# Optimization experiments

Measured on AMD Instinct MI355X. Metric: run time of the kernel, lower is better.

Reference implementation:

```python
import jax, jax.numpy as jnp
import numpy as np

B, SD, SE = 4, 2048, 2048
HID, HID_ = 300, 512
N_HEADS = 8


def setup_inputs() -> dict:
    key = jax.random.key(0)
    ks = jax.random.split(key, 7)
    en = jax.random.normal(ks[0], (B, SE, HID), dtype=jnp.float32)
    de = jax.random.normal(ks[1], (B, SD, HID), dtype=jnp.float32)
    mask = jax.random.randint(ks[2], (1, 1, SD, SE), 0, 2).astype(jnp.bool_)
    WQ = jax.random.normal(ks[3], (HID, HID_), dtype=jnp.float32)
    WK = jax.random.normal(ks[4], (HID, HID_), dtype=jnp.float32)
    WV = jax.random.normal(ks[5], (HID, HID_), dtype=jnp.float32)
    WO = jax.random.normal(ks[6], (HID_, HID), dtype=jnp.float32)
    return {"en": en, "de": de, "mask": mask, "WQ": WQ, "WK": WK, "WV": WV, "WO": WO}


def reference(en, de, mask, WQ, WK, WV, WO):
    # Faithful to the torch module (dropout in eval mode => identity).
    d_k = de.shape[-1]  # NOTE: original scales by sqrt(hidden_dim)=sqrt(300), not head_dim
    b_d, s_d = de.shape[0], de.shape[1]
    b_e, s_e = en.shape[0], en.shape[1]
    # head axis is the LAST axis of the reshape (size 8), exactly as the original view/permute
    q = jnp.transpose((de @ WQ).reshape(b_d, s_d, -1, N_HEADS), (3, 0, 1, 2))  # [8,B,Sd,64]
    k = jnp.transpose((en @ WK).reshape(b_e, s_e, -1, N_HEADS), (3, 0, 2, 1))  # [8,B,64,Se]
    v = jnp.transpose((en @ WV).reshape(b_e, s_e, -1, N_HEADS), (3, 0, 1, 2))  # [8,B,Se,64]
    e = jnp.matmul(q, k) / jnp.sqrt(jnp.asarray(d_k, dtype=q.dtype))           # [8,B,Sd,Se]
    e = jnp.where(mask, jnp.asarray(-1e9, dtype=e.dtype), e)
    alpha = jax.nn.softmax(e, axis=3)
    head3 = jnp.matmul(alpha, v)                                               # [8,B,Sd,64]
    # torch.cat((head3[0],...,head3[7]), 2) == move head axis into feature concat order
    a = jnp.concatenate([head3[h] for h in range(N_HEADS)], axis=2)            # [B,Sd,512]
    return a @ WO                                                              # [B,Sd,300]
```

## Files before the change

### kernel.cpp

```cpp
#include <hip/hip_runtime.h>
#include <hip/hip_bf16.h>
#include <math.h>

#define B_      4
#define SD_     2048
#define SE_     2048
#define HIDIN   300
#define HIDMID  512
#define NH      8
#define DH      64
#define ESZ     ((size_t)4194304)
#define BUFB    24576

typedef __attribute__((ext_vector_type(8))) short          s16x8;
typedef __attribute__((ext_vector_type(8))) unsigned short u16x8;
typedef __attribute__((ext_vector_type(4))) unsigned short u16x4;
typedef __attribute__((ext_vector_type(4))) float          f32x4;

#define MFMA16 __builtin_amdgcn_mfma_f32_16x16x32_bf16

#define QSCALE  0.0832940411f
#define NEGL   -1.4426950e9f
#define DEFER_THR 24.0f

__device__ __forceinline__ unsigned short f2bf(float f) {
    unsigned int u = __float_as_uint(f);
    u += 0x7fffu + ((u >> 16) & 1u);
    return (unsigned short)(u >> 16);
}
__device__ __forceinline__ float bf2f(unsigned short s) {
    return __uint_as_float((unsigned int)s << 16);
}
__device__ __forceinline__ void gload16(const void* g, void* l) {
    __builtin_amdgcn_global_load_lds(
        (const __attribute__((address_space(1))) void*)g,
        (__attribute__((address_space(3))) void*)l, 16, 0, 0);
}
__device__ __forceinline__ float fexp2(float x) {
#if __has_builtin(__builtin_amdgcn_exp2f)
    return __builtin_amdgcn_exp2f(x);
#else
    return exp2f(x);
#endif
}

#define OF_QH   ((size_t)0)
#define OF_QL   (ESZ)
#define OF_KH   (2*ESZ)
#define OF_KL   (3*ESZ)
#define OF_VT   (4*ESZ)
#define OF_CA   (5*ESZ)
#define OF_CW   (OF_CA + 10485760)
#define OF_WOT  (OF_CW + 983040)

__global__ __launch_bounds__(256) void bias_kernel(const int* __restrict__ mask,
                                                   unsigned int* __restrict__ BiasT)
{
    const int idx = blockIdx.x * 256 + threadIdx.x;
    const int q = idx >> 5, tile = idx & 31;
    const int* __restrict__ mrow = mask + (size_t)q * SE_ + tile * 64;
    const unsigned int NEGB = (unsigned int)f2bf(NEGL);
    const int qblk = q >> 4, qlo = q & 15;
#pragma unroll
    for (int g = 0; g < 4; ++g) {
        unsigned int w[8];
#pragma unroll
        for (int sub = 0; sub < 4; ++sub) {
            const int4 mm = *(const int4*)(mrow + sub * 16 + g * 4);
            w[sub * 2]     = (mm.x ? NEGB : 0u) | ((mm.y ? NEGB : 0u) << 16);
            w[sub * 2 + 1] = (mm.z ? NEGB : 0u) | ((mm.w ? NEGB : 0u) << 16);
        }
        unsigned int* dst = BiasT +
            ((((size_t)qblk * 32 + tile) * 4 + g) * 16 + qlo) * 8;
        *(uint4*)dst       = make_uint4(w[0], w[1], w[2], w[3]);
        *(uint4*)(dst + 4) = make_uint4(w[4], w[5], w[6], w[7]);
    }
}

__global__ __launch_bounds__(256) void convA_kernel(
    const float* __restrict__ de, const float* __restrict__ en,
    unsigned short* __restrict__ CA)
{
    const int idx = blockIdx.x * 256 + threadIdx.x;
    const int mat = blockIdx.y;
    const float* __restrict__ A = mat ? en : de;
    unsigned short* __restrict__ H = CA + (size_t)mat * 5242880;
    unsigned short* __restrict__ L = H + 2621440;
    const int row = idx / 10, ch = idx - row * 10;
    float v[32];
    if (ch < 9) {
#pragma unroll
        for (int i = 0; i < 8; ++i) {
            const float4 f = *(const float4*)(A + (size_t)row * 300 + ch * 32 + i * 4);
            v[i*4+0] = f.x; v[i*4+1] = f.y; v[i*4+2] = f.z; v[i*4+3] = f.w;
        }
    } else {
#pragma unroll
        for (int i = 0; i < 32; ++i) {
            const int k = 288 + i;
            v[i] = (k < 300) ? A[(size_t)row * 300 + k] : 0.f;
        }
    }
    const int r128 = row & 127;
    const int xr = (r128 >> 1) & 3;
    const size_t tb = ((size_t)(row >> 7) * 10 + ch) * 4096 + r128 * 32;
#pragma unroll
    for (int sub = 0; sub < 4; ++sub) {
        const int slot = sub ^ xr;
        u16x8 hv, lv;
#pragma unroll
        for (int e = 0; e < 8; ++e) {
            const float f = v[sub * 8 + e];
            const unsigned short h = f2bf(f);
            hv[e] = h; lv[e] = f2bf(f - bf2f(h));
        }
        *(u16x8*)(H + tb + slot * 8) = hv;
        *(u16x8*)(L + tb + slot * 8) = lv;
    }
}

__global__ __launch_bounds__(256) void convW_kernel(
    const float* __restrict__ WQ, const float* __restrict__ WK,
    const float* __restrict__ WV, const float* __restrict__ WO,
    unsigned short* __restrict__ CW, unsigned short* __restrict__ WOT)
{
    const int idx = blockIdx.x * 256 + threadIdx.x;
    if (idx < 122880) {
        const int which = idx / 40960;
        const int rem = idx - which * 40960;
        const int k = rem >> 7;
        const int n0 = (rem & 127) * 4;
        const float* __restrict__ W = which == 0 ? WQ : (which == 1 ? WK : WV);
        unsigned short* __restrict__ H = CW + (size_t)which * 327680;
        unsigned short* __restrict__ L = H + 163840;
        const float sc = (which == 0) ? QSCALE : 1.f;
        float4 w = make_float4(0.f, 0.f, 0.f, 0.f);
        if (k < 300) w = *(const float4*)(W + (size_t)k * 512 + n0);
        const float wv4[4] = {w.x * sc, w.y * sc, w.z * sc, w.w * sc};
        const int ch = k >> 5, kk = k & 31;
#pragma unroll
        for (int j = 0; j < 4; ++j) {
            const int n = n0 + j, ntile = n >> 7, nr = n & 127;
            const size_t o = ((size_t)(ntile * 10 + ch) * 128 + nr) * 32
                           + (((kk >> 3) ^ ((nr >> 1) & 3)) << 3) + (kk & 7);
            const unsigned short h = f2bf(wv4[j]);
            H[o] = h;
            if (which < 2) L[o] = f2bf(wv4[j] - bf2f(h));
        }
    } else {
        const int idx2 = idx - 122880;
        const int k = idx2 / 96, n4 = idx2 - k * 96;
        const int n0 = n4 * 4;
        float4 w = make_float4(0.f, 0.f, 0.f, 0.f);
        if (n0 < 300) w = *(const float4*)(WO + (size_t)k * 300 + n0);
        const float wv4[4] = {w.x, w.y, w.z, w.w};
        const int ch = k >> 5, kk = k & 31;
#pragma unroll
        for (int j = 0; j < 4; ++j) {
            const int n = n0 + j, ntile = n >> 7, nr = n & 127;
            const size_t o = ((size_t)(ntile * 16 + ch) * 128 + nr) * 32
                           + (((kk >> 3) ^ ((nr >> 1) & 3)) << 3) + (kk & 7);
            WOT[o] = f2bf(wv4[j]);
        }
    }
}

__global__ __launch_bounds__(256) void proj_qk_kernel(
    const unsigned short* __restrict__ CA, const unsigned short* __restrict__ CW,
    unsigned short* __restrict__ Qh, unsigned short* __restrict__ Ql,
    unsigned short* __restrict__ KhT, unsigned short* __restrict__ KlT)
{
    const int lin = blockIdx.x;
    const int which = lin >> 8;
    const int t = lin & 255;
    const int stile = (t & 7) | ((t >> 5) << 3);
    const int jtile = (t >> 3) & 3;
    const int tid = threadIdx.x, wv = tid >> 6, lane = tid & 63;
    const int li = lane & 15, g = lane >> 4;
    const int wr = wv >> 1, wc = wv & 1;

    __shared__ __align__(16) char LBp[65536];

    const unsigned short* __restrict__ pAh =
        CA + (size_t)which * 5242880 + (size_t)stile * 40960 + tid * 8;
    const unsigned short* __restrict__ pAl = pAh + 2621440;
    const unsigned short* __restrict__ pWh =
        CW + (size_t)which * 327680 + (size_t)jtile * 40960 + tid * 8;
    const unsigned short* __restrict__ pWl = pWh + 163840;

#define STAGEP(ch, bofs) {                                                    \
        char* db = LBp + (bofs) + wv * 1024;                                  \
        const size_t co = (size_t)(ch) * 4096;                                \
        gload16(pAh + co,        db);                                         \
        gload16(pAh + co + 2048, db + 4096);                                  \
        gload16(pAl + co,        db + 8192);                                  \
        gload16(pAl + co + 2048, db + 12288);                                 \
        gload16(pWh + co,        db + 16384);                                 \
        gload16(pWh + co + 2048, db + 20480);                                 \
        gload16(pWl + co,        db + 24576);                                 \
        gload16(pWl + co + 2048, db + 28672);                                 \
    }

    int offA[4], offW[4];
#pragma unroll
    for (int ssub = 0; ssub < 4; ++ssub) {
        const int r = wr * 64 + ssub * 16 + li;
        offA[ssub] = r * 64 + ((g ^ ((r >> 1) & 3)) << 4);
    }
#pragma unroll
    for (int jsub = 0; jsub < 4; ++jsub) {
        const int n = wc * 64 + jsub * 16 + li;
        offW[jsub] = n * 64 + ((g ^ ((n >> 1) & 3)) << 4);
    }

    f32x4 acc[4][4];
#pragma unroll
    for (int i = 0; i < 4; ++i)
#pragma unroll
        for (int j = 0; j < 4; ++j) acc[i][j] = (f32x4){0.f, 0.f, 0.f, 0.f};

    STAGEP(0, 0)
    __syncthreads();

#pragma unroll 1
    for (int ch = 0; ch < 10; ++ch) {
        const int bofs = (ch & 1) * 32768;
        if (ch < 9) STAGEP(ch + 1, bofs ^ 32768)
        const char* bp = LBp + bofs;
        s16x8 ah[4], al[4], wh[4], wl[4];
#pragma unroll
        for (int ssub = 0; ssub < 4; ++ssub) {
            ah[ssub] = *(const s16x8*)(bp + offA[ssub]);
            al[ssub] = *(const s16x8*)(bp + 8192 + offA[ssub]);
        }
#pragma unroll
        for (int jsub = 0; jsub < 4; ++jsub) {
            wh[jsub] = *(const s16x8*)(bp + 16384 + offW[jsub]);
            wl[jsub] = *(const s16x8*)(bp + 24576 + offW[jsub]);
        }
        __builtin_amdgcn_s_setprio(1);
#pragma unroll
        for (int ssub = 0; ssub < 4; ++ssub)
#pragma unroll
            for (int jsub = 0; jsub < 4; ++jsub) {
                acc[ssub][jsub] = MFMA16(ah[ssub], wh[jsub], acc[ssub][jsub], 0, 0, 0);
                acc[ssub][jsub] = MFMA16(ah[ssub], wl[jsub], acc[ssub][jsub], 0, 0, 0);
                acc[ssub][jsub] = MFMA16(al[ssub], wh[jsub], acc[ssub][jsub], 0, 0, 0);
            }
        __builtin_amdgcn_s_setprio(0);
        __syncthreads();
    }
#undef STAGEP

    const int jgbase = jtile * 128 + wc * 64 + li;
    const int sbase0 = stile * 128 + wr * 64 + 4 * g;
#pragma unroll
    for (int jsub = 0; jsub < 4; ++jsub) {
        const int jgg = jgbase + jsub * 16;
        const int d = jgg >> 3, hh = jgg & 7;
#pragma unroll
        for (int ssub = 0; ssub < 4; ++ssub) {
            const f32x4 v = acc[ssub][jsub];
            const int sg0 = sbase0 + ssub * 16;
            const int bbv = sg0 >> 11;
            const int bhn = bbv * 8 + hh;
            const int sl0 = sg0 & 2047;
            if (which == 0) {
                const size_t o = ((size_t)bhn * 2048 + sl0) * 64 + d;
#pragma unroll
                for (int r = 0; r < 4; ++r) {
                    const float val = v[r];
                    const unsigned short hi = f2bf(val);
                    Qh[o + r * 64] = hi;
                    Ql[o + r * 64] = f2bf(val - bf2f(hi));
                }
            } else {
                const int tile = sl0 >> 6, tt0 = sl0 & 63;
                const size_t tb = ((size_t)(bhn * 32 + tile)) << 12;
#pragma unroll
                for (int r = 0; r < 4; ++r) {
                    const int tt = tt0 + r;
                    const size_t o = tb + tt * 64 + (((d >> 3) ^ (tt & 7)) << 3) + (d & 7);
                    const float val = v[r];
                    const unsigned short hi = f2bf(val);
                    KhT[o] = hi;
                    KlT[o] = f2bf(val - bf2f(hi));
                }
            }
        }
    }
}

__global__ __launch_bounds__(256) void proj_v_kernel(
    const unsigned short* __restrict__ CA, const unsigned short* __restrict__ CW,
    unsigned short* __restrict__ VtT)
{
    const int t = blockIdx.x;
    const int stile = (t & 7) | ((t >> 5) << 3);
    const int jtile = (t >> 3) & 3;
    const int tid = threadIdx.x, wv = tid >> 6, lane = tid & 63;
    const int li = lane & 15, g = lane >> 4;
    const int wr = wv >> 1, wc = wv & 1;

    __shared__ __align__(16) char LBv[32768];

    const unsigned short* __restrict__ pAh =
        CA + (size_t)1 * 5242880 + (size_t)stile * 40960 + tid * 8;
    const unsigned short* __restrict__ pWh =
        CW + (size_t)2 * 327680 + (size_t)jtile * 40960 + tid * 8;

#define STAGEV(ch, bofs) {                                                    \
        char* db = LBv + (bofs) + wv * 1024;                                  \
        const size_t co = (size_t)(ch) * 4096;                                \
        gload16(pAh + co,        db);                                         \
        gload16(pAh + co + 2048, db + 4096);                                  \
        gload16(pWh + co,        db + 8192);                                  \
        gload16(pWh + co + 2048, db + 12288);                                 \
    }

    int offA[4], offW[4];
#pragma unroll
    for (int ssub = 0; ssub < 4; ++ssub) {
        const int r = wr * 64 + ssub * 16 + li;
        offA[ssub] = r * 64 + ((g ^ ((r >> 1) & 3)) << 4);
    }
#pragma unroll
    for (int jsub = 0; jsub < 4; ++jsub) {
        const int n = wc * 64 + jsub * 16 + li;
        offW[jsub] = 8192 + n * 64 + ((g ^ ((n >> 1) & 3)) << 4);
    }

    f32x4 acc[4][4];
#pragma unroll
    for (int i = 0; i < 4; ++i)
#pragma unroll
        for (int j = 0; j < 4; ++j) acc[i][j] = (f32x4){0.f, 0.f, 0.f, 0.f};

    STAGEV(0, 0)
    __syncthreads();

#pragma unroll 1
    for (int ch = 0; ch < 10; ++ch) {
        const int bofs = (ch & 1) * 16384;
        if (ch < 9) STAGEV(ch + 1, bofs ^ 16384)
        const char* bp = LBv + bofs;
        s16x8 ah[4], wh[4];
#pragma unroll
        for (int ssub = 0; ssub < 4; ++ssub)
            ah[ssub] = *(const s16x8*)(bp + offA[ssub]);
#pragma unroll
        for (int jsub = 0; jsub < 4; ++jsub)
            wh[jsub] = *(const s16x8*)(bp + offW[jsub]);
        __builtin_amdgcn_s_setprio(1);
#pragma unroll
        for (int ssub = 0; ssub < 4; ++ssub)
#pragma unroll
            for (int jsub = 0; jsub < 4; ++jsub)
                acc[ssub][jsub] = MFMA16(ah[ssub], wh[jsub], acc[ssub][jsub], 0, 0, 0);
        __builtin_amdgcn_s_setprio(0);
        __syncthreads();
    }
#undef STAGEV

    const int jgbase = jtile * 128 + wc * 64 + li;
    const int sbase0 = stile * 128 + wr * 64 + 4 * g;
#pragma unroll
    for (int jsub = 0; jsub < 4; ++jsub) {
        const int jgg = jgbase + jsub * 16;
        const int d = jgg >> 3, hh = jgg & 7;
#pragma unroll
        for (int ssub = 0; ssub < 4; ++ssub) {
            const f32x4 v = acc[ssub][jsub];
            const int sg0 = sbase0 + ssub * 16;
            const int bbv = sg0 >> 11;
            const int bhn = bbv * 8 + hh;
            const int sl0 = sg0 & 2047;
            const int tile = sl0 >> 6, tin0 = sl0 & 63;
            const size_t tb = ((size_t)(bhn * 32 + tile)) << 12;
            const int blk = tin0 >> 5, gg2 = (tin0 >> 2) & 3, half = (tin0 >> 4) & 1;
            const size_t o = tb + (size_t)d * 64
                           + ((((blk << 2) | gg2) ^ (d & 7)) << 3) + half * 4;
            u16x4 pk;
#pragma unroll
            for (int r = 0; r < 4; ++r) pk[r] = f2bf(v[r]);
            *(u16x4*)(VtT + o) = pk;
        }
    }
}

__global__ __launch_bounds__(512, 4) void attn_mfma_kernel(
    const unsigned short* __restrict__ Qh, const unsigned short* __restrict__ Ql,
    const unsigned short* __restrict__ KhT, const unsigned short* __restrict__ KlT,
    const unsigned short* __restrict__ VtT, const unsigned int* __restrict__ BiasT,
    unsigned short* __restrict__ AOb)
{
    const int lin = blockIdx.x + 16 * blockIdx.y;
    const int qt = (lin >> 3) & 15;
    const int bh = (lin & 7) + ((lin >> 7) << 3);
    const int bb = bh >> 3, hh = bh & 7;
    const int tid = threadIdx.x;
    const int wv = tid >> 6, lane = tid & 63;
    const int g = lane >> 4, li = lane & 15;
    const int q = qt * 128 + wv * 16 + li;

    __shared__ __align__(16) char LB[3 * BUFB];

    const size_t qoff = ((size_t)bh * SD_ + q) * DH + 8 * g;
    const s16x8 qh0 = *(const s16x8*)(Qh + qoff);
    const s16x8 qh1 = *(const s16x8*)(Qh + qoff + 32);
    const s16x8 ql0 = *(const s16x8*)(Ql + qoff);
    const s16x8 ql1 = *(const s16x8*)(Ql + qoff + 32);

    const unsigned short* __restrict__ sKh = KhT + ((size_t)bh << 17) + tid * 8;
    const unsigned short* __restrict__ sKl = KlT + ((size_t)bh << 17) + tid * 8;
    const unsigned short* __restrict__ sVt = VtT + ((size_t)bh << 17) + tid * 8;

    const int base0 = li * 128 + ((g ^ (li & 7)) << 4);
    const int base1 = li * 128 + (((4 + g) ^ (li & 7)) << 4);

    const size_t bbase = (size_t)(qt * 8 + wv) * 16384 + g * 128 + li * 8;

#define BIASLOAD(T, RA, RB) {                                                 \
        const uint4* p = (const uint4*)(BiasT + bbase + (size_t)(T) * 512);   \
        RA = p[0]; RB = p[1];                                                 \
    }

#define STAGE(tile, boff)                                                     \
    {                                                                         \
        char* db = LB + (boff) + wv * 1024;                                   \
        const size_t toff = (size_t)(tile) << 12;                             \
        gload16(sKh + toff, db);                                              \
        gload16(sKl + toff, db + 8192);                                       \
        gload16(sVt + toff, db + 16384);                                      \
    }

    float m = -INFINITY;
    f32x4 O[4], lacc;
#pragma unroll
    for (int i = 0; i < 4; ++i) O[i] = (f32x4){0.f, 0.f, 0.f, 0.f};
    lacc = (f32x4){0.f, 0.f, 0.f, 0.f};

    s16x8 ones;
#pragma unroll
    for (int i = 0; i < 8; ++i) ones[i] = (short)0x3F80;

    uint4 cBA, cBB, nBA, nBB;

#define UNPK(W, S, sub, cbase)                                                \
        S[sub][cbase]     = __uint_as_float((W) << 16);                       \
        S[sub][cbase + 1] = __uint_as_float((W) & 0xFFFF0000u);

#define ITER(IT, CBA_, CBB_, NBA_, NBB_)                                      \
    {                                                                         \
        BIASLOAD(((IT) + 1) & 31, NBA_, NBB_)                                 \
        STAGE(((IT) + 2) & 31, cs)                                            \
        f32x4 s[4];                                                           \
        UNPK(CBA_.x, s, 0, 0) UNPK(CBA_.y, s, 0, 2)                           \
        UNPK(CBA_.z, s, 1, 0) UNPK(CBA_.w, s, 1, 2)                           \
        UNPK(CBB_.x, s, 2, 0) UNPK(CBB_.y, s, 2, 2)                           \
        UNPK(CBB_.z, s, 3, 0) UNPK(CBB_.w, s, 3, 2)                           \
        __builtin_amdgcn_s_setprio(1);                                        \
        _Pragma("unroll")                                                     \
        for (int sub = 0; sub < 4; ++sub) {                                   \
            const s16x8 kh0 = *(const s16x8*)(LB + cc + base0 + sub * 2048);  \
            const s16x8 kh1 = *(const s16x8*)(LB + cc + base1 + sub * 2048);  \
            const s16x8 kl0 = *(const s16x8*)(LB + cc + base0 + 8192 + sub * 2048); \
            const s16x8 kl1 = *(const s16x8*)(LB + cc + base1 + 8192 + sub * 2048); \
            s[sub] = MFMA16(kh0, qh0, s[sub], 0, 0, 0);                       \
            s[sub] = MFMA16(kh0, ql0, s[sub], 0, 0, 0);                       \
            s[sub] = MFMA16(kl0, qh0, s[sub], 0, 0, 0);                       \
            s[sub] = MFMA16(kh1, qh1, s[sub], 0, 0, 0);                       \
            s[sub] = MFMA16(kh1, ql1, s[sub], 0, 0, 0);                       \
            s[sub] = MFMA16(kl1, qh1, s[sub], 0, 0, 0);                       \
        }                                                                     \
        __builtin_amdgcn_s_setprio(0);                                        \
        float x0 = fmaxf(fmaxf(s[0][0], s[0][1]), s[0][2]);                   \
        float x1 = fmaxf(fmaxf(s[0][3], s[1][0]), s[1][1]);                   \
        float x2 = fmaxf(fmaxf(s[1][2], s[1][3]), s[2][0]);                   \
        float x3 = fmaxf(fmaxf(s[2][1], s[2][2]), s[2][3]);                   \
        float x4 = fmaxf(fmaxf(s[3][0], s[3][1]), s[3][2]);                   \
        float tmax = fmaxf(fmaxf(fmaxf(x0, x1), fmaxf(x2, x3)),               \
                           fmaxf(x4, s[3][3]));                               \
        if (!__all(tmax <= m + DEFER_THR)) {                                  \
            float r = fmaxf(tmax, __shfl_xor(tmax, 16));                      \
            r = fmaxf(r, __shfl_xor(r, 32));                                  \
            const float mn  = fmaxf(m, r);                                    \
            const float scl = fexp2(m - mn);                                  \
            m = mn;                                                           \
            _Pragma("unroll")                                                 \
            for (int i = 0; i < 4; ++i) O[i] *= scl;                          \
            lacc *= scl;                                                      \
        }                                                                     \
        _Pragma("unroll")                                                     \
        for (int sub = 0; sub < 4; ++sub)                                     \
            _Pragma("unroll")                                                 \
            for (int c = 0; c < 4; ++c)                                       \
                s[sub][c] = fexp2(s[sub][c] - m);                             \
        union { s16x8 v; unsigned int w[4]; } P0, P1;                         \
        asm("v_cvt_pk_bf16_f32 %0, %1, %2" : "=v"(P0.w[0]) : "v"(s[0][0]), "v"(s[0][1])); \
        asm("v_cvt_pk_bf16_f32 %0, %1, %2" : "=v"(P0.w[1]) : "v"(s[0][2]), "v"(s[0][3])); \
        asm("v_cvt_pk_bf16_f32 %0, %1, %2" : "=v"(P0.w[2]) : "v"(s[1][0]), "v"(s[1][1])); \
        asm("v_cvt_pk_bf16_f32 %0, %1, %2" : "=v"(P0.w[3]) : "v"(s[1][2]), "v"(s[1][3])); \
        asm("v_cvt_pk_bf16_f32 %0, %1, %2" : "=v"(P1.w[0]) : "v"(s[2][0]), "v"(s[2][1])); \
        asm("v_cvt_pk_bf16_f32 %0, %1, %2" : "=v"(P1.w[1]) : "v"(s[2][2]), "v"(s[2][3])); \
        asm("v_cvt_pk_bf16_f32 %0, %1, %2" : "=v"(P1.w[2]) : "v"(s[3][0]), "v"(s[3][1])); \
        asm("v_cvt_pk_bf16_f32 %0, %1, %2" : "=v"(P1.w[3]) : "v"(s[3][2]), "v"(s[3][3])); \
        __builtin_amdgcn_s_setprio(1);                                        \
        _Pragma("unroll")                                                     \
        for (int dsub = 0; dsub < 4; ++dsub) {                                \
            const s16x8 vf0 = *(const s16x8*)(LB + cc + base0 + 16384 + dsub * 2048); \
            const s16x8 vf1 = *(const s16x8*)(LB + cc + base1 + 16384 + dsub * 2048); \
            O[dsub] = MFMA16(vf0, P0.v, O[dsub], 0, 0, 0);                    \
            O[dsub] = MFMA16(vf1, P1.v, O[dsub], 0, 0, 0);                    \
        }                                                                     \
        lacc = MFMA16(ones, P0.v, lacc, 0, 0, 0);                             \
        lacc = MFMA16(ones, P1.v, lacc, 0, 0, 0);                             \
        __builtin_amdgcn_s_setprio(0);                                        \
        asm volatile("s_waitcnt vmcnt(3)" ::: "memory");                      \
        __builtin_amdgcn_s_barrier();                                         \
        __builtin_amdgcn_sched_barrier(0);                                    \
        cc += BUFB; if (cc == 3 * BUFB) cc = 0;                               \
        cs += BUFB; if (cs == 3 * BUFB) cs = 0;                               \
    }

    int cc = 0, cs = 2 * BUFB;

    BIASLOAD(0, cBA, cBB)
    STAGE(0, 0)
    STAGE(1, BUFB)
    asm volatile("s_waitcnt vmcnt(3)" ::: "memory");
    __builtin_amdgcn_s_barrier();
    __builtin_amdgcn_sched_barrier(0);

#pragma unroll 1
    for (int it = 0; it < 32; it += 2) {
        ITER(it,     cBA, cBB, nBA, nBB)
        ITER(it + 1, nBA, nBB, cBA, cBB)
    }

    const float rl = 1.f / lacc[0];
    const int row = bb * 2048 + q;
    const int r128 = row & 127;
    const int xr = (r128 >> 1) & 3;
    unsigned short* __restrict__ ab = AOb + ((size_t)(row >> 7)) * 65536
                                    + r128 * 32 + (g & 1) * 4;
#pragma unroll
    for (int dsub = 0; dsub < 4; ++dsub) {
        const f32x4 o = O[dsub] * rl;
        const int ch = hh * 2 + (dsub >> 1);
        const int slot = ((dsub & 1) * 2 + (g >> 1)) ^ xr;
        u16x4 pk;
#pragma unroll
        for (int c = 0; c < 4; ++c) pk[c] = f2bf(o[c]);
        *(u16x4*)(ab + (size_t)ch * 4096 + slot * 8) = pk;
    }
#undef STAGE
#undef BIASLOAD
#undef UNPK
#undef ITER
}

__global__ __launch_bounds__(256) void epi_mfma_kernel(
    const unsigned short* __restrict__ AOb, const unsigned short* __restrict__ WOT,
    float* __restrict__ out)
{
    const int stile = blockIdx.x, jtile = blockIdx.y;
    const int tid = threadIdx.x, wv = tid >> 6, lane = tid & 63;
    const int li = lane & 15, g = lane >> 4;

    __shared__ __align__(16) char LBe[24576];

    const unsigned short* __restrict__ pA =
        AOb + (size_t)(stile >> 1) * 65536 + (stile & 1) * 2048 + tid * 8;
    const unsigned short* __restrict__ pW = WOT + (size_t)jtile * 65536 + tid * 8;

#define STAGEE(ch, bofs) {                                                    \
        char* dbA = LBe + (bofs) + wv * 1024;                                 \
        const size_t co = (size_t)(ch) * 4096;                                \
        gload16(pA + co,        dbA);                                         \
        gload16(pW + co,        dbA + 4096);                                  \
        gload16(pW + co + 2048, dbA + 8192);                                  \
    }

    int offA[4], offW[2];
#pragma unroll
    for (int ssub = 0; ssub < 4; ++ssub) {
        const int r = ssub * 16 + li;
        offA[ssub] = r * 64 + ((g ^ ((r >> 1) & 3)) << 4);
    }
#pragma unroll
    for (int jsub = 0; jsub < 2; ++jsub) {
        const int n = wv * 32 + jsub * 16 + li;
        offW[jsub] = 4096 + n * 64 + ((g ^ ((n >> 1) & 3)) << 4);
    }

    f32x4 acc[4][2];
#pragma unroll
    for (int i = 0; i < 4; ++i)
#pragma unroll
        for (int j = 0; j < 2; ++j) acc[i][j] = (f32x4){0.f, 0.f, 0.f, 0.f};

    STAGEE(0, 0)
    __syncthreads();

#pragma unroll 1
    for (int ch = 0; ch < 16; ++ch) {
        const int bofs = (ch & 1) * 12288;
        if (ch < 15) STAGEE(ch + 1, bofs ^ 12288)
        const char* bp = LBe + bofs;
        s16x8 ah[4], wh[2];
#pragma unroll
        for (int ssub = 0; ssub < 4; ++ssub)
            ah[ssub] = *(const s16x8*)(bp + offA[ssub]);
#pragma unroll
        for (int jsub = 0; jsub < 2; ++jsub)
            wh[jsub] = *(const s16x8*)(bp + offW[jsub]);
        __builtin_amdgcn_s_setprio(1);
#pragma unroll
        for (int ssub = 0; ssub < 4; ++ssub)
#pragma unroll
            for (int jsub = 0; jsub < 2; ++jsub)
                acc[ssub][jsub] = MFMA16(ah[ssub], wh[jsub], acc[ssub][jsub], 0, 0, 0);
        __builtin_amdgcn_s_setprio(0);
        __syncthreads();
    }
#undef STAGEE

    const int nbase = jtile * 128 + wv * 32 + li;
    const int rbase = stile * 64 + 4 * g;
#pragma unroll
    for (int jsub = 0; jsub < 2; ++jsub) {
        const int o = nbase + jsub * 16;
        if (o < HIDIN) {
#pragma unroll
            for (int ssub = 0; ssub < 4; ++ssub) {
                const f32x4 v = acc[ssub][jsub];
                const int r0 = rbase + ssub * 16;
#pragma unroll
                for (int r = 0; r < 4; ++r)
                    out[(size_t)(r0 + r) * HIDIN + o] = v[r];
            }
        }
    }
}

extern "C" void kernel_launch(void* const* d_in, const int* in_sizes, int n_in,
                              void* d_out, int out_size, void* d_ws, size_t ws_size,
                              hipStream_t stream)
{
    const float* en  = (const float*)d_in[0];
    const float* de  = (const float*)d_in[1];
    const int*   mask = (const int*)d_in[2];
    const float* WQ  = (const float*)d_in[3];
    const float* WK  = (const float*)d_in[4];
    const float* WV  = (const float*)d_in[5];
    const float* WO  = (const float*)d_in[6];
    float* out = (float*)d_out;

    unsigned short* ws2 = (unsigned short*)d_ws;
    unsigned short* Qh  = ws2 + OF_QH;
    unsigned short* Ql  = ws2 + OF_QL;
    unsigned short* KhT = ws2 + OF_KH;
    unsigned short* KlT = ws2 + OF_KL;
    unsigned short* VtT = ws2 + OF_VT;
    unsigned short* CA  = ws2 + OF_CA;
    unsigned short* CW  = ws2 + OF_CW;
    unsigned short* WOT = ws2 + OF_WOT;
    unsigned short* AOb = CA;
    unsigned int*  BiasT = (unsigned int*)(CA + 4194304);

    convA_kernel<<<dim3(320, 2), 256, 0, stream>>>(de, en, CA);
    convW_kernel<<<dim3(672), 256, 0, stream>>>(WQ, WK, WV, WO, CW, WOT);
    proj_qk_kernel<<<dim3(512), 256, 0, stream>>>(CA, CW, Qh, Ql, KhT, KlT);
    proj_v_kernel<<<dim3(256), 256, 0, stream>>>(CA, CW, VtT);
    bias_kernel<<<dim3(256), 256, 0, stream>>>(mask, BiasT);
    attn_mfma_kernel<<<dim3(16, 32), 512, 0, stream>>>(Qh, Ql, KhT, KlT, VtT, BiasT, AOb);
    epi_mfma_kernel<<<dim3(128, 3), 256, 0, stream>>>(AOb, WOT, out);
}
```

Baseline: 176.0 us.

## Split attention over key range with two query rows per wave and merge pass

Adds an attention kernel that splits the key sequence into two halves across blocks. Each wave processes two 16-row query groups, so every K/V tile loaded into LDS feeds twice the MFMA work. The kernel writes partial outputs plus per-row max and sum to workspace, and a new merge kernel combines them into the blocked layout that the epilogue kernel expects. In exchange, each wave holds more registers, partial results make an extra round trip through memory, and the path needs a larger workspace, falling back to the original kernel when the workspace is too small.

```diff
diff --git a/kernel.cpp b/kernel.cpp
--- a/kernel.cpp
+++ b/kernel.cpp
@@ -52,6 +52,8 @@
 #define OF_CA   (5*ESZ)
 #define OF_CW   (OF_CA + 10485760)
 #define OF_WOT  (OF_CW + 983040)
+#define OF_PART (OF_WOT + 196608)
+#define WS_NEED_SPLIT ((size_t)(OF_PART + 8388608 + 524288) * 2)
 
 __global__ __launch_bounds__(256) void bias_kernel(const int* __restrict__ mask,
                                                    unsigned int* __restrict__ BiasT)
@@ -424,7 +426,6 @@
         const uint4* p = (const uint4*)(BiasT + bbase + (size_t)(T) * 512);   \
         RA = p[0]; RB = p[1];                                                 \
     }
-
 #define STAGE(tile, boff)                                                     \
     {                                                                         \
         char* db = LB + (boff) + wv * 1024;                                   \
@@ -560,6 +561,252 @@
 #undef ITER
 }
 
+__global__ __launch_bounds__(512, 4) void attn2_kernel(
+    const unsigned short* __restrict__ Qh, const unsigned short* __restrict__ Ql,
+    const unsigned short* __restrict__ KhT, const unsigned short* __restrict__ KlT,
+    const unsigned short* __restrict__ VtT, const unsigned int* __restrict__ BiasT,
+    unsigned short* __restrict__ Opart, float2* __restrict__ ML)
+{
+    const int lin = blockIdx.x + 16 * blockIdx.y;
+    const int qt2 = (lin >> 3) & 15;
+    const int qt = qt2 >> 1, split = qt2 & 1;
+    const int bh = (lin & 7) | ((lin >> 7) << 3);
+    const int tid = threadIdx.x;
+    const int wv = tid >> 6, lane = tid & 63;
+    const int g = lane >> 4, li = lane & 15;
+    const int q0 = qt * 256 + wv * 16 + li;
+    const int tbase = split * 16;
+
+    __shared__ __align__(16) char LB[3 * BUFB];
+
+    const size_t qoff = ((size_t)bh * SD_ + q0) * DH + 8 * g;
+    const s16x8 qh0_0 = *(const s16x8*)(Qh + qoff);
+    const s16x8 qh1_0 = *(const s16x8*)(Qh + qoff + 32);
+    const s16x8 ql0_0 = *(const s16x8*)(Ql + qoff);
+    const s16x8 ql1_0 = *(const s16x8*)(Ql + qoff + 32);
+    const s16x8 qh0_1 = *(const s16x8*)(Qh + qoff + 8192);
+    const s16x8 qh1_1 = *(const s16x8*)(Qh + qoff + 8224);
+    const s16x8 ql0_1 = *(const s16x8*)(Ql + qoff + 8192);
+    const s16x8 ql1_1 = *(const s16x8*)(Ql + qoff + 8224);
+
+    const unsigned short* __restrict__ sKh = KhT + ((size_t)bh << 17) + tid * 8;
+    const unsigned short* __restrict__ sKl = KlT + ((size_t)bh << 17) + tid * 8;
+    const unsigned short* __restrict__ sVt = VtT + ((size_t)bh << 17) + tid * 8;
+
+    const int base0 = li * 128 + ((g ^ (li & 7)) << 4);
+    const int base1 = li * 128 + (((4 + g) ^ (li & 7)) << 4);
+
+    const size_t bb0 = (size_t)(qt * 16 + wv) * 16384 + g * 128 + li * 8;
+    const size_t bb1 = bb0 + 131072;
+
+#define STAGE2(tile, boff)                                                    \
+    {                                                                         \
+        char* db = LB + (boff) + wv * 1024;                                   \
+        const size_t toff = (size_t)(tile) << 12;                             \
+        gload16(sKh + toff, db);                                              \
+        gload16(sKl + toff, db + 8192);                                       \
+        gload16(sVt + toff, db + 16384);                                      \
+    }
+#define UNPK2(W, S, sub, cbase)                                               \
+        S[sub][cbase]     = __uint_as_float((W) << 16);                       \
+        S[sub][cbase + 1] = __uint_as_float((W) & 0xFFFF0000u);
+
+    float m0 = -INFINITY, m1 = -INFINITY;
+    f32x4 O0[4], O1[4], lacc0, lacc1;
+#pragma unroll
+    for (int i = 0; i < 4; ++i) {
+        O0[i] = (f32x4){0.f, 0.f, 0.f, 0.f};
+        O1[i] = (f32x4){0.f, 0.f, 0.f, 0.f};
+    }
+    lacc0 = (f32x4){0.f, 0.f, 0.f, 0.f};
+    lacc1 = (f32x4){0.f, 0.f, 0.f, 0.f};
+
+    s16x8 ones;
+#pragma unroll
+    for (int i = 0; i < 8; ++i) ones[i] = (short)0x3F80;
+
+    int cc = 0, cs = 2 * BUFB;
+    STAGE2(tbase, 0)
+    STAGE2(tbase + 1, BUFB)
+    asm volatile("s_waitcnt vmcnt(3)" ::: "memory");
+    __builtin_amdgcn_s_barrier();
+    __builtin_amdgcn_sched_barrier(0);
+
+#pragma unroll 1
+    for (int it = 0; it < 16; ++it) {
+        const uint4* pb0 = (const uint4*)(BiasT + bb0 + (size_t)(tbase + it) * 512);
+        const uint4 bA0 = pb0[0], bB0 = pb0[1];
+        const uint4* pb1 = (const uint4*)(BiasT + bb1 + (size_t)(tbase + it) * 512);
+        const uint4 bA1 = pb1[0], bB1 = pb1[1];
+        STAGE2(tbase + ((it + 2) & 15), cs)
+
+        f32x4 s0[4], s1[4];
+        UNPK2(bA0.x, s0, 0, 0) UNPK2(bA0.y, s0, 0, 2)
+        UNPK2(bA0.z, s0, 1, 0) UNPK2(bA0.w, s0, 1, 2)
+        UNPK2(bB0.x, s0, 2, 0) UNPK2(bB0.y, s0, 2, 2)
+        UNPK2(bB0.z, s0, 3, 0) UNPK2(bB0.w, s0, 3, 2)
+        UNPK2(bA1.x, s1, 0, 0) UNPK2(bA1.y, s1, 0, 2)
+        UNPK2(bA1.z, s1, 1, 0) UNPK2(bA1.w, s1, 1, 2)
+        UNPK2(bB1.x, s1, 2, 0) UNPK2(bB1.y, s1, 2, 2)
+        UNPK2(bB1.z, s1, 3, 0) UNPK2(bB1.w, s1, 3, 2)
+
+        __builtin_amdgcn_s_setprio(1);
+#pragma unroll
+        for (int sub = 0; sub < 4; ++sub) {
+            const s16x8 kh0 = *(const s16x8*)(LB + cc + base0 + sub * 2048);
+            const s16x8 kh1 = *(const s16x8*)(LB + cc + base1 + sub * 2048);
+            const s16x8 kl0 = *(const s16x8*)(LB + cc + base0 + 8192 + sub * 2048);
+            const s16x8 kl1 = *(const s16x8*)(LB + cc + base1 + 8192 + sub * 2048);
+            s0[sub] = MFMA16(kh0, qh0_0, s0[sub], 0, 0, 0);
+            s0[sub] = MFMA16(kh0, ql0_0, s0[sub], 0, 0, 0);
+            s0[sub] = MFMA16(kl0, qh0_0, s0[sub], 0, 0, 0);
+            s0[sub] = MFMA16(kh1, qh1_0, s0[sub], 0, 0, 0);
+            s0[sub] = MFMA16(kh1, ql1_0, s0[sub], 0, 0, 0);
+            s0[sub] = MFMA16(kl1, qh1_0, s0[sub], 0, 0, 0);
+            s1[sub] = MFMA16(kh0, qh0_1, s1[sub], 0, 0, 0);
+            s1[sub] = MFMA16(kh0, ql0_1, s1[sub], 0, 0, 0);
+            s1[sub] = MFMA16(kl0, qh0_1, s1[sub], 0, 0, 0);
+            s1[sub] = MFMA16(kh1, qh1_1, s1[sub], 0, 0, 0);
+            s1[sub] = MFMA16(kh1, ql1_1, s1[sub], 0, 0, 0);
+            s1[sub] = MFMA16(kl1, qh1_1, s1[sub], 0, 0, 0);
+        }
+        __builtin_amdgcn_s_setprio(0);
+
+        float t0, t1;
+        {
+            float a = fmaxf(fmaxf(s0[0][0], s0[0][1]), s0[0][2]);
+            float b = fmaxf(fmaxf(s0[0][3], s0[1][0]), s0[1][1]);
+            float c = fmaxf(fmaxf(s0[1][2], s0[1][3]), s0[2][0]);
+            float d = fmaxf(fmaxf(s0[2][1], s0[2][2]), s0[2][3]);
+            float e = fmaxf(fmaxf(s0[3][0], s0[3][1]), s0[3][2]);
+            t0 = fmaxf(fmaxf(fmaxf(a, b), fmaxf(c, d)), fmaxf(e, s0[3][3]));
+        }
+        {
+            float a = fmaxf(fmaxf(s1[0][0], s1[0][1]), s1[0][2]);
+            float b = fmaxf(fmaxf(s1[0][3], s1[1][0]), s1[1][1]);
+            float c = fmaxf(fmaxf(s1[1][2], s1[1][3]), s1[2][0]);
+            float d = fmaxf(fmaxf(s1[2][1], s1[2][2]), s1[2][3]);
+            float e = fmaxf(fmaxf(s1[3][0], s1[3][1]), s1[3][2]);
+            t1 = fmaxf(fmaxf(fmaxf(a, b), fmaxf(c, d)), fmaxf(e, s1[3][3]));
+        }
+        const int okd = (t0 <= m0 + DEFER_THR) && (t1 <= m1 + DEFER_THR);
+        if (!__all(okd)) {
+            float r0 = fmaxf(t0, __shfl_xor(t0, 16));
+            r0 = fmaxf(r0, __shfl_xor(r0, 32));
+            float r1 = fmaxf(t1, __shfl_xor(t1, 16));
+            r1 = fmaxf(r1, __shfl_xor(r1, 32));
+            const float mn0 = fmaxf(m0, r0), mn1 = fmaxf(m1, r1);
+            const float sc0 = fexp2(m0 - mn0), sc1 = fexp2(m1 - mn1);
+            m0 = mn0; m1 = mn1;
+#pragma unroll
+            for (int i = 0; i < 4; ++i) { O0[i] *= sc0; O1[i] *= sc1; }
+            lacc0 *= sc0; lacc1 *= sc1;
+        }
+#pragma unroll
+        for (int sub = 0; sub < 4; ++sub)
+#pragma unroll
+            for (int c = 0; c < 4; ++c) {
+                s0[sub][c] = fexp2(s0[sub][c] - m0);
+                s1[sub][c] = fexp2(s1[sub][c] - m1);
+            }
+
+        union { s16x8 v; unsigned int w[4]; } P00, P10, P01, P11;
+        asm("v_cvt_pk_bf16_f32 %0, %1, %2" : "=v"(P00.w[0]) : "v"(s0[0][0]), "v"(s0[0][1]));
+        asm("v_cvt_pk_bf16_f32 %0, %1, %2" : "=v"(P00.w[1]) : "v"(s0[0][2]), "v"(s0[0][3]));
+        asm("v_cvt_pk_bf16_f32 %0, %1, %2" : "=v"(P00.w[2]) : "v"(s0[1][0]), "v"(s0[1][1]));
+        asm("v_cvt_pk_bf16_f32 %0, %1, %2" : "=v"(P00.w[3]) : "v"(s0[1][2]), "v"(s0[1][3]));
+        asm("v_cvt_pk_bf16_f32 %0, %1, %2" : "=v"(P10.w[0]) : "v"(s0[2][0]), "v"(s0[2][1]));
+        asm("v_cvt_pk_bf16_f32 %0, %1, %2" : "=v"(P10.w[1]) : "v"(s0[2][2]), "v"(s0[2][3]));
+        asm("v_cvt_pk_bf16_f32 %0, %1, %2" : "=v"(P10.w[2]) : "v"(s0[3][0]), "v"(s0[3][1]));
+        asm("v_cvt_pk_bf16_f32 %0, %1, %2" : "=v"(P10.w[3]) : "v"(s0[3][2]), "v"(s0[3][3]));
+        asm("v_cvt_pk_bf16_f32 %0, %1, %2" : "=v"(P01.w[0]) : "v"(s1[0][0]), "v"(s1[0][1]));
+        asm("v_cvt_pk_bf16_f32 %0, %1, %2" : "=v"(P01.w[1]) : "v"(s1[0][2]), "v"(s1[0][3]));
+        asm("v_cvt_pk_bf16_f32 %0, %1, %2" : "=v"(P01.w[2]) : "v"(s1[1][0]), "v"(s1[1][1]));
+        asm("v_cvt_pk_bf16_f32 %0, %1, %2" : "=v"(P01.w[3]) : "v"(s1[1][2]), "v"(s1[1][3]));
+        asm("v_cvt_pk_bf16_f32 %0, %1, %2" : "=v"(P11.w[0]) : "v"(s1[2][0]), "v"(s1[2][1]));
+        asm("v_cvt_pk_bf16_f32 %0, %1, %2" : "=v"(P11.w[1]) : "v"(s1[2][2]), "v"(s1[2][3]));
+        asm("v_cvt_pk_bf16_f32 %0, %1, %2" : "=v"(P11.w[2]) : "v"(s1[3][0]), "v"(s1[3][1]));
+        asm("v_cvt_pk_bf16_f32 %0, %1, %2" : "=v"(P11.w[3]) : "v"(s1[3][2]), "v"(s1[3][3]));
+
+        __builtin_amdgcn_s_setprio(1);
+#pragma unroll
+        for (int dsub = 0; dsub < 4; ++dsub) {
+            const s16x8 vf0 = *(const s16x8*)(LB + cc + base0 + 16384 + dsub * 2048);
+            const s16x8 vf1 = *(const s16x8*)(LB + cc + base1 + 16384 + dsub * 2048);
+            O0[dsub] = MFMA16(vf0, P00.v, O0[dsub], 0, 0, 0);
+            O0[dsub] = MFMA16(vf1, P10.v, O0[dsub], 0, 0, 0);
+            O1[dsub] = MFMA16(vf0, P01.v, O1[dsub], 0, 0, 0);
+            O1[dsub] = MFMA16(vf1, P11.v, O1[dsub], 0, 0, 0);
+        }
+        lacc0 = MFMA16(ones, P00.v, lacc0, 0, 0, 0);
+        lacc0 = MFMA16(ones, P10.v, lacc0, 0, 0, 0);
+        lacc1 = MFMA16(ones, P01.v, lacc1, 0, 0, 0);
+        lacc1 = MFMA16(ones, P11.v, lacc1, 0, 0, 0);
+        __builtin_amdgcn_s_setprio(0);
+
+        asm volatile("s_waitcnt vmcnt(3)" ::: "memory");
+        __builtin_amdgcn_s_barrier();
+        __builtin_amdgcn_sched_barrier(0);
+        cc += BUFB; if (cc == 3 * BUFB) cc = 0;
+        cs += BUFB; if (cs == 3 * BUFB) cs = 0;
+    }
+
+#pragma unroll
+    for (int qs = 0; qs < 2; ++qs) {
+        const int qr = qt * 256 + qs * 128 + wv * 16 + li;
+        const f32x4* Oq = qs ? O1 : O0;
+        const float mq = qs ? m1 : m0;
+        const float lq = qs ? lacc1[0] : lacc0[0];
+        unsigned short* pb = Opart + ((size_t)(split * 32 + bh) * 2048 + qr) * 64;
+#pragma unroll
+        for (int dsub = 0; dsub < 4; ++dsub) {
+            u16x4 pk;
+#pragma unroll
+            for (int c = 0; c < 4; ++c) pk[c] = f2bf(Oq[dsub][c]);
+            *(u16x4*)(pb + dsub * 16 + 4 * g) = pk;
+        }
+        if (g == 0)
+            ML[(size_t)split * 65536 + (size_t)bh * 2048 + qr] = make_float2(mq, lq);
+    }
+#undef STAGE2
+#undef UNPK2
+}
+
+__global__ __launch_bounds__(256) void merge_kernel(
+    const unsigned short* __restrict__ Opart, const float2* __restrict__ ML,
+    unsigned short* __restrict__ AOb)
+{
+    const int idx = blockIdx.x * 256 + threadIdx.x;
+    const int bh = idx >> 11, q = idx & 2047;
+    const float2 a = ML[idx];
+    const float2 b = ML[65536 + idx];
+    const float M = fmaxf(a.x, b.x);
+    const float s0 = fexp2(a.x - M), s1 = fexp2(b.x - M);
+    const float l = a.y * s0 + b.y * s1;
+    const float w0 = s0 / l, w1 = s1 / l;
+    const unsigned short* p0 = Opart + (size_t)idx * 64;
+    const unsigned short* p1 = p0 + 4194304;
+
+    const int bb = bh >> 3, hh = bh & 7;
+    const int row = bb * 2048 + q;
+    const int r128 = row & 127;
+    const int xr = (r128 >> 1) & 3;
+    unsigned short* __restrict__ ab = AOb + ((size_t)(row >> 7)) * 65536 + r128 * 32;
+#pragma unroll
+    for (int d0 = 0; d0 < 64; d0 += 4) {
+        const u16x4 x = *(const u16x4*)(p0 + d0);
+        const u16x4 y = *(const u16x4*)(p1 + d0);
+        u16x4 o;
+#pragma unroll
+        for (int c = 0; c < 4; ++c)
+            o[c] = f2bf(bf2f(x[c]) * w0 + bf2f(y[c]) * w1);
+        const int dsub = d0 >> 4, gq = (d0 >> 2) & 3;
+        const int ch = hh * 2 + (dsub >> 1);
+        const int slot = ((dsub & 1) * 2 + (gq >> 1)) ^ xr;
+        *(u16x4*)(ab + (gq & 1) * 4 + (size_t)ch * 4096 + slot * 8) = o;
+    }
+}
+
 __global__ __launch_bounds__(256) void epi_mfma_kernel(
     const unsigned short* __restrict__ AOb, const unsigned short* __restrict__ WOT,
     float* __restrict__ out)
@@ -674,6 +921,16 @@
     proj_qk_kernel<<<dim3(512), 256, 0, stream>>>(CA, CW, Qh, Ql, KhT, KlT);
     proj_v_kernel<<<dim3(256), 256, 0, stream>>>(CA, CW, VtT);
     bias_kernel<<<dim3(256), 256, 0, stream>>>(mask, BiasT);
-    attn_mfma_kernel<<<dim3(16, 32), 512, 0, stream>>>(Qh, Ql, KhT, KlT, VtT, BiasT, AOb);
+
+    if (ws_size >= WS_NEED_SPLIT) {
+        unsigned short* Opart = ws2 + OF_PART;
+        float2* ML = (float2*)(ws2 + OF_PART + 8388608);
+        attn2_kernel<<<dim3(16, 32), 512, 0, stream>>>(Qh, Ql, KhT, KlT, VtT,
+                                                       BiasT, Opart, ML);
+        merge_kernel<<<dim3(256), 256, 0, stream>>>(Opart, ML, AOb);
+    } else {
+        attn_mfma_kernel<<<dim3(16, 32), 512, 0, stream>>>(Qh, Ql, KhT, KlT, VtT,
+                                                           BiasT, AOb);
+    }
     epi_mfma_kernel<<<dim3(128, 3), 256, 0, stream>>>(AOb, WOT, out);
 }
```

New measurement: 205.8 us. 17.0% more time.
